# Kernel optimization log

Hardware: AMD Instinct MI355X
Metric: run time of the kernel (lower is better)

## Reference

```python
import jax, jax.numpy as jnp
import numpy as np

B, S, D, H = 2, 2048, 1024, 16
DK = D // H
EPS = 1e-5


def setup_inputs() -> dict:
    key = jax.random.key(0)
    ks = jax.random.split(key, 6)
    std = (2.0 / (D + D)) ** 0.5
    return {
        "x": jax.random.normal(ks[0], (B, S, D), dtype=jnp.float32),
        "W_Q": jax.random.normal(ks[1], (D, D), dtype=jnp.float32) * std,
        "W_K": jax.random.normal(ks[2], (D, D), dtype=jnp.float32) * std,
        "W_V": jax.random.normal(ks[3], (D, D), dtype=jnp.float32) * std,
        "W_O": jax.random.normal(ks[4], (D, D), dtype=jnp.float32) * std,
        "gain": jnp.ones((D,), dtype=jnp.float32),
        "positions": jnp.arange(S, dtype=jnp.int64 if jax.config.jax_enable_x64 else jnp.int32),
        "theta": 10000,
        "max_seq_len": 2048,
    }


def rmsnorm(x, gain):
    xf = x.astype(jnp.float32)
    rms = jnp.sqrt(jnp.mean(xf * xf, axis=-1, keepdims=True) + EPS)
    return ((xf / rms) * gain).astype(x.dtype)


def apply_rope(x, sin, cos):
    # x: [..., seq, dk]; sin/cos: [seq, dk//2] broadcast over leading dims
    x_even = x[..., 0::2]
    x_odd = x[..., 1::2]
    r_even = x_even * cos - x_odd * sin
    r_odd = x_odd * cos + x_even * sin
    return jnp.stack([r_even, r_odd], axis=-1).reshape(x.shape)


def reference(x, W_Q, W_K, W_V, W_O, gain, positions, theta, max_seq_len):
    seq_len = x.shape[-2]
    Q = jnp.einsum('od,bsd->bso', W_Q, x)
    K = jnp.einsum('od,bsd->bso', W_K, x)
    V = jnp.einsum('od,bsd->bso', W_V, x)
    # RMSNorm over full d_model BEFORE head split (as in original)
    Q = rmsnorm(Q, gain)
    K = rmsnorm(K, gain)
    # split heads: [b, h, s, dk]
    Q = Q.reshape(*Q.shape[:-1], H, DK).swapaxes(-3, -2)
    K = K.reshape(*K.shape[:-1], H, DK).swapaxes(-3, -2)
    V = V.reshape(*V.shape[:-1], H, DK).swapaxes(-3, -2)
    # RoPE tables
    exponents = 2.0 * jnp.arange(DK // 2, dtype=jnp.float32) / DK
    inv_freq = 1.0 / (jnp.float32(theta) ** exponents)
    angles = positions.astype(jnp.float32)[:, None] * inv_freq[None, :]  # [S, DK//2]
    sin, cos = jnp.sin(angles), jnp.cos(angles)
    Q = apply_rope(Q, sin, cos)
    K = apply_rope(K, sin, cos)
    # causal attention
    scores = jnp.einsum('bhqd,bhkd->bhqk', Q, K) / jnp.sqrt(jnp.float32(DK))
    causal = jnp.tril(jnp.ones((seq_len, seq_len), dtype=bool))
    scores = jnp.where(causal, scores, -jnp.inf)
    attn = jax.nn.softmax(scores, axis=-1)
    out = jnp.einsum('bhqk,bhkd->bhqd', attn, V)
    out = out.swapaxes(-3, -2).reshape(*x.shape[:-1], D)
    return jnp.einsum('of,bsf->bso', W_O, out)
```

## Files before the change

### kernel.cpp

```cpp
#include <hip/hip_runtime.h>
#include <hip/hip_bf16.h>

typedef __attribute__((ext_vector_type(8))) __bf16 bf16x8;
typedef __attribute__((ext_vector_type(4))) __bf16 bf16x4;
typedef __attribute__((ext_vector_type(4))) float  f32x4;
typedef __attribute__((ext_vector_type(4))) short  s16x4;

#define S_LEN 2048
#define D_DIM 1024
#define NH    16
#define GK    1024
#define GN    1024

__device__ __forceinline__ float fast_exp2(float x) {
#if __has_builtin(__builtin_amdgcn_exp2f)
  return __builtin_amdgcn_exp2f(x);
#else
  return exp2f(x);
#endif
}

__device__ __forceinline__ f32x4 mfma16(bf16x4 a, bf16x4 b, f32x4 c) {
#if __has_builtin(__builtin_amdgcn_mfma_f32_16x16x16_bf16)
  return __builtin_amdgcn_mfma_f32_16x16x16_bf16(a, b, c, 0, 0, 0);
#else
  return __builtin_amdgcn_mfma_f32_16x16x16bf16_1k(
      __builtin_bit_cast(s16x4, a), __builtin_bit_cast(s16x4, b), c, 0, 0, 0);
#endif
}

__device__ __forceinline__ void gld_lds16(const void* g, void* l) {
  __builtin_amdgcn_global_load_lds(
      (const __attribute__((address_space(1))) unsigned int*)g,
      (__attribute__((address_space(3))) unsigned int*)l, 16, 0, 0);
}

__global__ __launch_bounds__(256) void cast_all(
    const float* __restrict__ x,  const float* __restrict__ wq, const float* __restrict__ wk,
    const float* __restrict__ wv, const float* __restrict__ wo,
    __bf16* __restrict__ xb, __bf16* __restrict__ wqb, __bf16* __restrict__ wkb,
    __bf16* __restrict__ wvb, __bf16* __restrict__ wob)
{
  const int NTOT = 2 << 20;
  for (int i = blockIdx.x * 256 + threadIdx.x; i < NTOT; i += 1024 * 256) {
    const float* s; __bf16* d; int off;
    if (i < (1 << 20)) { s = x; d = xb; off = i; }
    else {
      const int j = i - (1 << 20);
      const int r = j >> 18; off = j & ((1 << 18) - 1);
      s = (r == 0) ? wq : (r == 1) ? wk : (r == 2) ? wv : wo;
      d = (r == 0) ? wqb : (r == 1) ? wkb : (r == 2) ? wvb : wob;
    }
    float4 v = ((const float4*)s)[off];
    bf16x4 o = { (__bf16)v.x, (__bf16)v.y, (__bf16)v.z, (__bf16)v.w };
    ((bf16x4*)d)[off] = o;
  }
}

__global__ __launch_bounds__(256, 3) void gemm_qkv(
    const __bf16* __restrict__ A,
    const __bf16* __restrict__ W0, const __bf16* __restrict__ W1, const __bf16* __restrict__ W2,
    __bf16* __restrict__ C0, __bf16* __restrict__ C1, __bf16* __restrict__ VtOut)
{
  const int bid = blockIdx.x;
  const int e = bid & 7, mg = e >> 1, ng = e & 1;
  const int q = bid >> 3;
  const int mt = mg * 8 + (q & 7);
  const int nt = ng * 12 + (q >> 3);
  const int mode = nt >> 3;
  const int m0 = mt * 128;
  const int n0 = (nt & 7) * 128;
  const __bf16* Wm = (mode == 0) ? W0 : (mode == 1) ? W1 : W2;

  __shared__ __align__(16) __bf16 As[128 * 64];
  __shared__ __align__(16) __bf16 Bs[128 * 64];

  const int tid  = threadIdx.x;
  const int lane = tid & 63;
  const int w    = tid >> 6;
  const int wr   = w >> 1, wc = w & 1;
  const int lm   = lane & 15, qd = lane >> 4;

  const __bf16* ap[4]; int loA[4];
  #pragma unroll
  for (int j = 0; j < 4; j++) {
    const int c = tid + 256 * j;
    const int r = c >> 3, cpos = c & 7;
    ap[j] = A + (size_t)(m0 + r) * GK + (cpos ^ (r & 7)) * 8;
    loA[j] = c * 8;
  }
  const __bf16* bp[4]; int loB[4];
  #pragma unroll
  for (int j = 0; j < 4; j++) {
    const int c = tid + 256 * j;
    const int r = c >> 3, cpos = c & 7;
    bp[j] = Wm + (size_t)(n0 + r) * GK + (cpos ^ (r & 7)) * 8;
    loB[j] = c * 8;
  }

  const int sw = lm & 7;

  f32x4 zero = {0.f, 0.f, 0.f, 0.f};
  f32x4 acc[4][4];
  #pragma unroll
  for (int i = 0; i < 4; i++)
    #pragma unroll
    for (int j = 0; j < 4; j++) acc[i][j] = zero;

  for (int k0 = 0; k0 < GK; k0 += 64) {
    #pragma unroll
    for (int j = 0; j < 4; j++) gld_lds16(ap[j] + k0, &As[loA[j]]);
    #pragma unroll
    for (int j = 0; j < 4; j++) gld_lds16(bp[j] + k0, &Bs[loB[j]]);
    __syncthreads();
    #pragma unroll
    for (int half = 0; half < 2; half++) {
      const int cph = ((qd + 4 * half) ^ sw) * 8;
      bf16x8 af[4], bfv[4];
      #pragma unroll
      for (int i = 0; i < 4; i++) af[i]  = *(const bf16x8*)&As[(wr * 64 + i * 16 + lm) * 64 + cph];
      #pragma unroll
      for (int j = 0; j < 4; j++) bfv[j] = *(const bf16x8*)&Bs[(wc * 64 + j * 16 + lm) * 64 + cph];
      #pragma unroll
      for (int i = 0; i < 4; i++)
        #pragma unroll
        for (int j = 0; j < 4; j++)
          acc[i][j] = __builtin_amdgcn_mfma_f32_16x16x32_bf16(af[i], bfv[j], acc[i][j], 0, 0, 0);
    }
    __syncthreads();
  }

  if (mode < 2) {
    __bf16* C = (mode == 0) ? C0 : C1;
    #pragma unroll
    for (int i = 0; i < 4; i++) {
      const int row = m0 + wr * 64 + i * 16 + qd * 4;
      #pragma unroll
      for (int j = 0; j < 4; j++) {
        const int col = n0 + wc * 64 + j * 16 + lm;
        #pragma unroll
        for (int r = 0; r < 4; r++)
          C[(size_t)(row + r) * GN + col] = (__bf16)acc[i][j][r];
      }
    }
  } else {
    #pragma unroll
    for (int i = 0; i < 4; i++) {
      const int row = m0 + wr * 64 + i * 16 + qd * 4;
      const int b = row >> 11, s = row & (S_LEN - 1);
      #pragma unroll
      for (int j = 0; j < 4; j++) {
        const int col = n0 + wc * 64 + j * 16 + lm;
        const int h = col >> 6, d = col & 63;
        bf16x4 o = { (__bf16)acc[i][j][0], (__bf16)acc[i][j][1],
                     (__bf16)acc[i][j][2], (__bf16)acc[i][j][3] };
        *(bf16x4*)(VtOut + (((size_t)(b * NH + h) * 64 + d) * S_LEN + s)) = o;
      }
    }
  }
}

__global__ __launch_bounds__(256, 2) void gemm_out64(
    const __bf16* __restrict__ A, const __bf16* __restrict__ Wm, float* __restrict__ C)
{
  const int bid = blockIdx.x;
  const int e = bid & 7, mg = e >> 1, ng = e & 1;
  const int q = bid >> 3;
  const int m0 = (mg * 16 + (q & 15)) * 64;
  const int n0 = (ng * 4 + (q >> 4)) * 128;

  __shared__ __align__(16) __bf16 As[2][64 * 64];
  __shared__ __align__(16) __bf16 Bs[2][128 * 64];

  const int tid  = threadIdx.x;
  const int lane = tid & 63;
  const int w    = tid >> 6;
  const int wr   = w >> 1, wc = w & 1;
  const int lm   = lane & 15, qd = lane >> 4;

  const __bf16* ap[2]; int loA[2];
  #pragma unroll
  for (int j = 0; j < 2; j++) {
    const int c = tid + 256 * j;
    const int r = c >> 3, cpos = c & 7;
    ap[j] = A + (size_t)(m0 + r) * GK + (cpos ^ (r & 7)) * 8;
    loA[j] = c * 8;
  }
  const __bf16* bp[4]; int loB[4];
  #pragma unroll
  for (int j = 0; j < 4; j++) {
    const int c = tid + 256 * j;
    const int r = c >> 3, cpos = c & 7;
    bp[j] = Wm + (size_t)(n0 + r) * GK + (cpos ^ (r & 7)) * 8;
    loB[j] = c * 8;
  }

  const int sw = lm & 7;

  auto stage = [&](int buf, int k0) {
    #pragma unroll
    for (int j = 0; j < 2; j++) gld_lds16(ap[j] + k0, &As[buf][loA[j]]);
    #pragma unroll
    for (int j = 0; j < 4; j++) gld_lds16(bp[j] + k0, &Bs[buf][loB[j]]);
  };

  f32x4 zero = {0.f, 0.f, 0.f, 0.f};
  f32x4 acc[2][4];
  #pragma unroll
  for (int i = 0; i < 2; i++)
    #pragma unroll
    for (int j = 0; j < 4; j++) acc[i][j] = zero;

  stage(0, 0);

  for (int kt = 0; kt < 16; ++kt) {
    const int cur = kt & 1;
    __syncthreads();
    if (kt < 15) stage(cur ^ 1, (kt + 1) * 64);
    #pragma unroll
    for (int half = 0; half < 2; half++) {
      const int cph = ((qd + 4 * half) ^ sw) * 8;
      bf16x8 af[2], bfv[4];
      #pragma unroll
      for (int i = 0; i < 2; i++) af[i]  = *(const bf16x8*)&As[cur][(wr * 32 + i * 16 + lm) * 64 + cph];
      #pragma unroll
      for (int j = 0; j < 4; j++) bfv[j] = *(const bf16x8*)&Bs[cur][(wc * 64 + j * 16 + lm) * 64 + cph];
      #pragma unroll
      for (int i = 0; i < 2; i++)
        #pragma unroll
        for (int j = 0; j < 4; j++)
          acc[i][j] = __builtin_amdgcn_mfma_f32_16x16x32_bf16(af[i], bfv[j], acc[i][j], 0, 0, 0);
    }
  }

  #pragma unroll
  for (int i = 0; i < 2; i++) {
    const int row = m0 + wr * 32 + i * 16 + qd * 4;
    #pragma unroll
    for (int j = 0; j < 4; j++) {
      const int col = n0 + wc * 64 + j * 16 + lm;
      #pragma unroll
      for (int r = 0; r < 4; r++)
        C[(size_t)(row + r) * GN + col] = acc[i][j][r];
    }
  }
}

__global__ __launch_bounds__(256) void norm_rope(
    const __bf16* __restrict__ Qf, const __bf16* __restrict__ Kf,
    const float* __restrict__ gain, const int* __restrict__ positions,
    const int* __restrict__ theta_p,
    __bf16* __restrict__ Qh, __bf16* __restrict__ Kh)
{
  const int t = threadIdx.x;
  const int w = t >> 6, lane = t & 63;
  const int row = blockIdx.x * 4 + w;
  const int s = row & (S_LEN - 1), b = row >> 11;
  const int d0 = lane * 16;

  const bf16x8 qv0 = *(const bf16x8*)(Qf + (size_t)row * D_DIM + d0);
  const bf16x8 qv1 = *(const bf16x8*)(Qf + (size_t)row * D_DIM + d0 + 8);
  const bf16x8 kv0 = *(const bf16x8*)(Kf + (size_t)row * D_DIM + d0);
  const bf16x8 kv1 = *(const bf16x8*)(Kf + (size_t)row * D_DIM + d0 + 8);

  float q[16], k[16];
  #pragma unroll
  for (int j = 0; j < 8; j++) {
    q[j] = (float)qv0[j]; q[8 + j] = (float)qv1[j];
    k[j] = (float)kv0[j]; k[8 + j] = (float)kv1[j];
  }
  float sq = 0.f, sk = 0.f;
  #pragma unroll
  for (int j = 0; j < 16; j++) { sq += q[j] * q[j]; sk += k[j] * k[j]; }
  #pragma unroll
  for (int off = 32; off; off >>= 1) { sq += __shfl_xor(sq, off); sk += __shfl_xor(sk, off); }

  const float SC2 = 0.125f * 1.44269504089f;
  const float invq = rsqrtf(sq * (1.0f / 1024.0f) + 1e-5f) * SC2;
  const float invk = rsqrtf(sk * (1.0f / 1024.0f) + 1e-5f);

  float g[16];
  #pragma unroll
  for (int j = 0; j < 4; j++) {
    const float4 gv = *(const float4*)(gain + d0 + j * 4);
    g[4 * j] = gv.x; g[4 * j + 1] = gv.y; g[4 * j + 2] = gv.z; g[4 * j + 3] = gv.w;
  }

  const float pos  = (float)positions[s];
  const float lg32 = __log2f((float)theta_p[0]) * (1.0f / 32.0f);
  const int h = lane >> 2, idx0 = (lane & 3) * 16;

  bf16x8 qw0, qw1, kw0, kw1;
  #pragma unroll
  for (int pp = 0; pp < 8; pp++) {
    const int p = (lane & 3) * 8 + pp;
    const float f = fast_exp2(-(float)p * lg32);
    float sn, cs;
    __sincosf(pos * f, &sn, &cs);
    const float qe = q[2 * pp] * invq * g[2 * pp];
    const float qo = q[2 * pp + 1] * invq * g[2 * pp + 1];
    const float ke = k[2 * pp] * invk * g[2 * pp];
    const float ko = k[2 * pp + 1] * invk * g[2 * pp + 1];
    const __bf16 qre = (__bf16)(qe * cs - qo * sn);
    const __bf16 qro = (__bf16)(qo * cs + qe * sn);
    const __bf16 kre = (__bf16)(ke * cs - ko * sn);
    const __bf16 kro = (__bf16)(ko * cs + ke * sn);
    if (pp < 4) { qw0[2 * pp] = qre; qw0[2 * pp + 1] = qro;
                  kw0[2 * pp] = kre; kw0[2 * pp + 1] = kro; }
    else        { qw1[2 * (pp - 4)] = qre; qw1[2 * (pp - 4) + 1] = qro;
                  kw1[2 * (pp - 4)] = kre; kw1[2 * (pp - 4) + 1] = kro; }
  }

  const size_t obase = ((size_t)((b * NH + h) * S_LEN + s)) * 64 + idx0;
  *(bf16x8*)(Qh + obase)     = qw0;
  *(bf16x8*)(Qh + obase + 8) = qw1;
  *(bf16x8*)(Kh + obase)     = kw0;
  *(bf16x8*)(Kh + obase + 8) = kw1;
}

__global__ __launch_bounds__(256) void attn_fwd(
    const __bf16* __restrict__ Qh, const __bf16* __restrict__ Kh,
    const __bf16* __restrict__ Vt, __bf16* __restrict__ Ob)
{
  const int bid = blockIdx.x;
  const int g   = bid >> 5, gj = g & 7, gs = g >> 3;
  const int qt  = (gs == 0) ? 31 - gj : (gs == 1) ? gj : (gs == 2) ? 23 - gj : 8 + gj;
  const int rr  = bid & 31;
  const int bh  = (rr & 7) * 4 + (rr >> 3);
  const int tid = threadIdx.x, lane = tid & 63, w = tid >> 6;
  const int lm = lane & 15, qd = lane >> 4;

  __shared__ __align__(16) __bf16 smem[8192 + 8192];
  __bf16* Ks = smem;
  __bf16* Vs = smem + 8192;

  const int row0 = qt * 64 + w * 16;
  const int qglob = row0 + lm;
  const size_t qbase = (size_t)bh * S_LEN * 64;
  const bf16x8 aq0 = *(const bf16x8*)(Qh + qbase + (size_t)qglob * 64 + qd * 8);
  const bf16x8 aq1 = *(const bf16x8*)(Qh + qbase + (size_t)qglob * 64 + 32 + qd * 8);

  const __bf16* Kb = Kh + (size_t)bh * S_LEN * 64;
  const __bf16* Vb = Vt + (size_t)bh * 64 * S_LEN;
  const int c0 = tid, c1 = 256 + tid;
  const int kr0 = c0 >> 3, kr1 = c1 >> 3;
  const int kg0 = ((c0 & 7) ^ (kr0 & 7)) * 8;
  const int kg1 = ((c1 & 7) ^ (kr1 & 7)) * 8;
  const int cpA = (qd ^ (lm & 7)) * 8;
  const int cpB = cpA ^ 32;

  auto stage = [&](int buf, int k0) {
    __bf16* Kd = Ks + buf * 4096;
    __bf16* Vd = Vs + buf * 4096;
    gld_lds16(Kb + (size_t)(k0 + kr0) * 64 + kg0, &Kd[c0 * 8]);
    gld_lds16(Kb + (size_t)(k0 + kr1) * 64 + kg1, &Kd[c1 * 8]);
    gld_lds16(Vb + (size_t)kr0 * S_LEN + k0 + kg0, &Vd[c0 * 8]);
    gld_lds16(Vb + (size_t)kr1 * S_LEN + k0 + kg1, &Vd[c1 * 8]);
  };

  f32x4 zero = {0.f, 0.f, 0.f, 0.f};
  f32x4 lacc = zero;
  f32x4 o[4];
  #pragma unroll
  for (int jb = 0; jb < 4; jb++) o[jb] = zero;

  bf16x4 ones4;
  #pragma unroll
  for (int i = 0; i < 4; i++) ones4[i] = (__bf16)1.0f;

  stage(0, 0);

  for (int kt = 0; kt <= qt; ++kt) {
    const int cur = kt & 1;
    __syncthreads();
    if (kt < qt) stage(cur ^ 1, (kt + 1) * 64);

    const __bf16* Kc = Ks + cur * 4096;
    const __bf16* Vc = Vs + cur * 4096;
    const int k0 = kt * 64;
    const bool diag = (kt == qt);

    bf16x4 pfrag[4];
    #pragma unroll
    for (int kb = 0; kb < 4; kb++) {
      const int krow = (kb * 16 + lm) * 64;
      const bf16x8 ak0 = *(const bf16x8*)&Kc[krow + cpA];
      const bf16x8 ak1 = *(const bf16x8*)&Kc[krow + cpB];
      f32x4 sc = zero;
      sc = __builtin_amdgcn_mfma_f32_16x16x32_bf16(ak0, aq0, sc, 0, 0, 0);
      sc = __builtin_amdgcn_mfma_f32_16x16x32_bf16(ak1, aq1, sc, 0, 0, 0);
      float p[4];
      if (diag) {
        const int keyb = k0 + kb * 16 + qd * 4;
        #pragma unroll
        for (int r = 0; r < 4; r++)
          p[r] = (keyb + r <= qglob) ? fast_exp2(sc[r]) : 0.f;
      } else {
        #pragma unroll
        for (int r = 0; r < 4; r++) p[r] = fast_exp2(sc[r]);
      }
      bf16x4 pf = { (__bf16)p[0], (__bf16)p[1], (__bf16)p[2], (__bf16)p[3] };
      pfrag[kb] = pf;
      lacc = mfma16(ones4, pf, lacc);
    }

    #pragma unroll
    for (int jb = 0; jb < 4; jb++) {
      const int vrow = jb * 16 + lm;
      const int rsw = vrow & 7;
      #pragma unroll
      for (int kb = 0; kb < 4; kb++) {
        const int c = 2 * kb + (qd >> 1);
        const bf16x4 av = *(const bf16x4*)&Vc[vrow * 64 + ((c ^ rsw) << 3) + (qd & 1) * 4];
        o[jb] = mfma16(av, pfrag[kb], o[jb]);
      }
    }
  }

  const int b = bh >> 4, h = bh & 15;
  const float inv = 1.0f / lacc[0];
  const size_t base = ((size_t)(b * S_LEN + qglob)) * D_DIM + h * 64 + qd * 4;
  #pragma unroll
  for (int jb = 0; jb < 4; jb++) {
    bf16x4 ov = { (__bf16)(o[jb][0] * inv), (__bf16)(o[jb][1] * inv),
                  (__bf16)(o[jb][2] * inv), (__bf16)(o[jb][3] * inv) };
    *(bf16x4*)(Ob + base + jb * 16) = ov;
  }
}

extern "C" void kernel_launch(void* const* d_in, const int* in_sizes, int n_in,
                              void* d_out, int out_size, void* d_ws, size_t ws_size,
                              hipStream_t stream)
{
  (void)in_sizes; (void)n_in; (void)out_size; (void)ws_size;
  const float* x    = (const float*)d_in[0];
  const float* WQ   = (const float*)d_in[1];
  const float* WK   = (const float*)d_in[2];
  const float* WV   = (const float*)d_in[3];
  const float* WO   = (const float*)d_in[4];
  const float* gain = (const float*)d_in[5];
  const int* positions = (const int*)d_in[6];
  const int* theta     = (const int*)d_in[7];
  float* out = (float*)d_out;

  char* ws = (char*)d_ws;
  const size_t MB = 1024 * 1024;
  __bf16* xb  = (__bf16*)(ws + 0);
  __bf16* WQb = (__bf16*)(ws + 8  * MB);
  __bf16* WKb = (__bf16*)(ws + 10 * MB);
  __bf16* WVb = (__bf16*)(ws + 12 * MB);
  __bf16* WOb = (__bf16*)(ws + 14 * MB);
  __bf16* Qfb = (__bf16*)(ws + 16 * MB);
  __bf16* Kfb = (__bf16*)(ws + 24 * MB);
  __bf16* Vt  = (__bf16*)(ws + 32 * MB);
  __bf16* Qh  = (__bf16*)(ws + 40 * MB);
  __bf16* Kh  = (__bf16*)(ws + 48 * MB);
  __bf16* Ob  = (__bf16*)(ws + 56 * MB);

  cast_all<<<1024, 256, 0, stream>>>(x, WQ, WK, WV, WO, xb, WQb, WKb, WVb, WOb);
  gemm_qkv<<<768, 256, 0, stream>>>(xb, WQb, WKb, WVb, Qfb, Kfb, Vt);
  norm_rope<<<1024, 256, 0, stream>>>(Qfb, Kfb, gain, positions, theta, Qh, Kh);
  attn_fwd<<<1024, 256, 0, stream>>>(Qh, Kh, Vt, Ob);
  gemm_out64<<<512, 256, 0, stream>>>(Ob, WOb, out);
}
```

Before: 180.5 us.

## Store V in MFMA-fragment order and load it directly into registers

The QKV GEMM epilogue now writes V in a pre-swizzled layout that matches the per-lane B-operand fragment of the 16x16x16 MFMA. The attention kernel then reads V tiles straight from global memory into registers, with no LDS staging, and shared memory holds only the K double buffer. Launch bounds are raised to 4 blocks per CU. This removes the LDS traffic and footprint for V in exchange for uncoalesced-latency global loads issued every K-tile that are not prefetched ahead, plus extra register pressure from holding 16 V fragments.

```diff
diff --git a/kernel.cpp b/kernel.cpp
--- a/kernel.cpp
+++ b/kernel.cpp
@@ -148,13 +148,18 @@
     for (int i = 0; i < 4; i++) {
       const int row = m0 + wr * 64 + i * 16 + qd * 4;
       const int b = row >> 11, s = row & (S_LEN - 1);
+      const int kt = s >> 6, kb = (s >> 4) & 3, qp = (s >> 2) & 3;
       #pragma unroll
       for (int j = 0; j < 4; j++) {
         const int col = n0 + wc * 64 + j * 16 + lm;
         const int h = col >> 6, d = col & 63;
+        const int jb = d >> 4, lmv = d & 15;
         bf16x4 o = { (__bf16)acc[i][j][0], (__bf16)acc[i][j][1],
                      (__bf16)acc[i][j][2], (__bf16)acc[i][j][3] };
-        *(bf16x4*)(VtOut + (((size_t)(b * NH + h) * 64 + d) * S_LEN + s)) = o;
+        const size_t idx =
+            ((((size_t)((b * NH + h) * 32 + kt)) * 4 + kb) * 4 + jb) * 256 +
+            (qp * 16 + lmv) * 4;
+        *(bf16x4*)(VtOut + idx) = o;
       }
     }
   }
@@ -318,9 +323,9 @@
   *(bf16x8*)(Kh + obase + 8) = kw1;
 }
 
-__global__ __launch_bounds__(256) void attn_fwd(
+__global__ __launch_bounds__(256, 4) void attn_fwd(
     const __bf16* __restrict__ Qh, const __bf16* __restrict__ Kh,
-    const __bf16* __restrict__ Vt, __bf16* __restrict__ Ob)
+    const __bf16* __restrict__ Vf, __bf16* __restrict__ Ob)
 {
   const int bid = blockIdx.x;
   const int g   = bid >> 5, gj = g & 7, gs = g >> 3;
@@ -330,9 +335,7 @@
   const int tid = threadIdx.x, lane = tid & 63, w = tid >> 6;
   const int lm = lane & 15, qd = lane >> 4;
 
-  __shared__ __align__(16) __bf16 smem[8192 + 8192];
-  __bf16* Ks = smem;
-  __bf16* Vs = smem + 8192;
+  __shared__ __align__(16) __bf16 Ks[2][4096];
 
   const int row0 = qt * 64 + w * 16;
   const int qglob = row0 + lm;
@@ -341,7 +344,7 @@
   const bf16x8 aq1 = *(const bf16x8*)(Qh + qbase + (size_t)qglob * 64 + 32 + qd * 8);
 
   const __bf16* Kb = Kh + (size_t)bh * S_LEN * 64;
-  const __bf16* Vb = Vt + (size_t)bh * 64 * S_LEN;
+  const __bf16* Vbh = Vf + (size_t)bh * 32 * 4096;
   const int c0 = tid, c1 = 256 + tid;
   const int kr0 = c0 >> 3, kr1 = c1 >> 3;
   const int kg0 = ((c0 & 7) ^ (kr0 & 7)) * 8;
@@ -350,12 +353,8 @@
   const int cpB = cpA ^ 32;
 
   auto stage = [&](int buf, int k0) {
-    __bf16* Kd = Ks + buf * 4096;
-    __bf16* Vd = Vs + buf * 4096;
-    gld_lds16(Kb + (size_t)(k0 + kr0) * 64 + kg0, &Kd[c0 * 8]);
-    gld_lds16(Kb + (size_t)(k0 + kr1) * 64 + kg1, &Kd[c1 * 8]);
-    gld_lds16(Vb + (size_t)kr0 * S_LEN + k0 + kg0, &Vd[c0 * 8]);
-    gld_lds16(Vb + (size_t)kr1 * S_LEN + k0 + kg1, &Vd[c1 * 8]);
+    gld_lds16(Kb + (size_t)(k0 + kr0) * 64 + kg0, &Ks[buf][c0 * 8]);
+    gld_lds16(Kb + (size_t)(k0 + kr1) * 64 + kg1, &Ks[buf][c1 * 8]);
   };
 
   f32x4 zero = {0.f, 0.f, 0.f, 0.f};
@@ -375,8 +374,15 @@
     __syncthreads();
     if (kt < qt) stage(cur ^ 1, (kt + 1) * 64);
 
-    const __bf16* Kc = Ks + cur * 4096;
-    const __bf16* Vc = Vs + cur * 4096;
+    const __bf16* Vtile = Vbh + (size_t)kt * 4096;
+    bf16x4 av[4][4];
+    #pragma unroll
+    for (int kb = 0; kb < 4; kb++)
+      #pragma unroll
+      for (int jb = 0; jb < 4; jb++)
+        av[kb][jb] = *(const bf16x4*)(Vtile + ((kb * 4 + jb) * 64 + lane) * 4);
+
+    const __bf16* Kc = &Ks[cur][0];
     const int k0 = kt * 64;
     const bool diag = (kt == qt);
 
@@ -405,16 +411,10 @@
     }
 
     #pragma unroll
-    for (int jb = 0; jb < 4; jb++) {
-      const int vrow = jb * 16 + lm;
-      const int rsw = vrow & 7;
-      #pragma unroll
-      for (int kb = 0; kb < 4; kb++) {
-        const int c = 2 * kb + (qd >> 1);
-        const bf16x4 av = *(const bf16x4*)&Vc[vrow * 64 + ((c ^ rsw) << 3) + (qd & 1) * 4];
-        o[jb] = mfma16(av, pfrag[kb], o[jb]);
-      }
-    }
+    for (int jb = 0; jb < 4; jb++)
+      #pragma unroll
+      for (int kb = 0; kb < 4; kb++)
+        o[jb] = mfma16(av[kb][jb], pfrag[kb], o[jb]);
   }
 
   const int b = bh >> 4, h = bh & 15;
@@ -452,14 +452,14 @@
   __bf16* WOb = (__bf16*)(ws + 14 * MB);
   __bf16* Qfb = (__bf16*)(ws + 16 * MB);
   __bf16* Kfb = (__bf16*)(ws + 24 * MB);
-  __bf16* Vt  = (__bf16*)(ws + 32 * MB);
+  __bf16* Vf  = (__bf16*)(ws + 32 * MB);
   __bf16* Qh  = (__bf16*)(ws + 40 * MB);
   __bf16* Kh  = (__bf16*)(ws + 48 * MB);
   __bf16* Ob  = (__bf16*)(ws + 56 * MB);
 
   cast_all<<<1024, 256, 0, stream>>>(x, WQ, WK, WV, WO, xb, WQb, WKb, WVb, WOb);
-  gemm_qkv<<<768, 256, 0, stream>>>(xb, WQb, WKb, WVb, Qfb, Kfb, Vt);
+  gemm_qkv<<<768, 256, 0, stream>>>(xb, WQb, WKb, WVb, Qfb, Kfb, Vf);
   norm_rope<<<1024, 256, 0, stream>>>(Qfb, Kfb, gain, positions, theta, Qh, Kh);
-  attn_fwd<<<1024, 256, 0, stream>>>(Qh, Kh, Vt, Ob);
+  attn_fwd<<<1024, 256, 0, stream>>>(Qh, Kh, Vf, Ob);
   gemm_out64<<<512, 256, 0, stream>>>(Ob, WOb, out);
 }
```

Measured after the change: 192.2 us. 1.06x slower.
